# Kernel tuning notes

Hardware: AMD Instinct MI355X
Metric: run time of the kernel (lower is better)

The kernel has to match this reference:

```python
import jax, jax.numpy as jnp
import numpy as np

N_HEADS = 16


def _rope_table(seq_len, head_dim):
    # Matches RotaryPositionalEmbedding: emb = cat(sin(pos*inv_freq), cos(pos*inv_freq))
    inv_freq = 1.0 / (10000.0 ** (jnp.arange(0, head_dim, 2, dtype=jnp.float32) / head_dim))
    sinusoid = jnp.arange(seq_len, dtype=jnp.float32)[:, None] * inv_freq[None, :]  # [S, hd/2]
    return jnp.sin(sinusoid), jnp.cos(sinusoid)


def _apply_rope(q, k, seq_len, head_dim):
    # Faithful to the torch code, which slices emb[:, :hd/2] (== sin) and calls it 'cos',
    # and emb[:, hd/2:] (== cos) and calls it 'sin'. We keep that exact math.
    sin_tab, cos_tab = _rope_table(seq_len, head_dim)
    c = sin_tab[None, None]  # named 'cos' in torch code, actually sin values
    s = cos_tab[None, None]  # named 'sin' in torch code, actually cos values
    half = head_dim // 2
    def rot(x):
        x1, x2 = x[..., :half], x[..., half:]
        return jnp.concatenate([x1 * c - x2 * s, x2 * c + x1 * s], axis=-1)
    return rot(q), rot(k)


def setup_inputs() -> dict:
    key = jax.random.key(0)
    ks = jax.random.split(key, 9)
    B, S, D = 4, 2048, 1024
    sc = 1.0 / np.sqrt(D)
    return {
        'hidden_states': jax.random.normal(ks[0], (B, S, D), jnp.float32),
        'Wq': jax.random.normal(ks[1], (D, D), jnp.float32) * sc,
        'bq': jax.random.normal(ks[2], (D,), jnp.float32) * 0.01,
        'Wk': jax.random.normal(ks[3], (D, D), jnp.float32) * sc,
        'bk': jax.random.normal(ks[4], (D,), jnp.float32) * 0.01,
        'Wv': jax.random.normal(ks[5], (D, D), jnp.float32) * sc,
        'bv': jax.random.normal(ks[6], (D,), jnp.float32) * 0.01,
        'Wo': jax.random.normal(ks[7], (D, D), jnp.float32) * sc,
        'bo': jax.random.normal(ks[8], (D,), jnp.float32) * 0.01,
    }


def reference(hidden_states, Wq, bq, Wk, bk, Wv, bv, Wo, bo):
    B, S, D = hidden_states.shape
    H = N_HEADS
    hd = D // H

    def proj(W, b):
        y = jnp.einsum('bsd,ed->bse', hidden_states, W) + b  # nn.Linear: x @ W.T + b
        return y.reshape(B, S, H, hd).transpose(0, 2, 1, 3)   # [B,H,S,hd]

    q = proj(Wq, bq)
    k = proj(Wk, bk)
    v = proj(Wv, bv)
    q, k = _apply_rope(q, k, S, hd)

    scale = 1.0 / np.sqrt(hd)
    scores = jnp.einsum('bhqd,bhkd->bhqk', q, k) * scale  # [B,H,S,S]
    attn = jax.nn.softmax(scores, axis=-1)
    ctx = jnp.einsum('bhqk,bhkd->bhqd', attn, v)          # [B,H,S,hd]
    ctx = ctx.transpose(0, 2, 1, 3).reshape(B, S, D)
    return jnp.einsum('bsd,ed->bse', ctx, Wo) + bo
```

## Files before the change

kernel.cpp:

```cpp
#include <hip/hip_runtime.h>
#include <math.h>

#define SEQ 2048
#define DMODEL 1024
#define NH 16
#define HD 64
#define BH 64
#define MROWS 8192
#define QKV_U16 8388608
#define LOG2E 1.4426950408889634f

typedef __attribute__((ext_vector_type(8))) _Float16 half8;
typedef __attribute__((ext_vector_type(4))) _Float16 half4;
typedef __attribute__((ext_vector_type(2))) __fp16 fp16v2;
typedef __attribute__((ext_vector_type(8))) short short8;
typedef __attribute__((ext_vector_type(4))) float floatx4;
typedef unsigned short ush;

union FH { _Float16 h; ush u; };
union PK { fp16v2 v; unsigned u; };
union PH { unsigned u[2]; half4 h; };

__device__ inline ush f2h(float x) { FH c; c.h = (_Float16)x; return c.u; }

__device__ inline void glds16(const ush* g, ush* l) {
  __builtin_amdgcn_global_load_lds((const __attribute__((address_space(1))) void*)g,
                                   (__attribute__((address_space(3))) void*)l, 16, 0, 0);
}

__global__ __launch_bounds__(256)
void cvt_kb(const float* __restrict__ src, ush* __restrict__ dst, int M) {
  __shared__ float T[64][33];
  const int t = threadIdx.x;
  const int k0 = blockIdx.x * 32, m0 = blockIdx.y * 64;
  {
    int row = t >> 2, c = (t & 3) * 8;
    const float* sp = src + (size_t)(m0 + row) * DMODEL + k0 + c;
    float4 x0 = *(const float4*)sp;
    float4 x1 = *(const float4*)(sp + 4);
    float xs[8] = {x0.x, x0.y, x0.z, x0.w, x1.x, x1.y, x1.z, x1.w};
#pragma unroll
    for (int j = 0; j < 8; ++j) T[row][c + j] = xs[j];
  }
  __syncthreads();
  const int ml = t & 63, kbl = t >> 6;
  short8 h8;
#pragma unroll
  for (int j = 0; j < 8; ++j) h8[j] = (short)f2h(T[ml][kbl * 8 + j]);
  *(short8*)(dst + ((size_t)(k0 / 8 + kbl) * M + m0 + ml) * 8) = h8;
}

__global__ __launch_bounds__(256)
void cvt_w4(const float* __restrict__ W0, const float* __restrict__ W1,
            const float* __restrict__ W2, const float* __restrict__ W3,
            ush* __restrict__ dst, float2* __restrict__ tab) {
  __shared__ float T[64][33];
  const int z = blockIdx.z;
  if (z == 3) {
    const int idx = (blockIdx.y * 32 + blockIdx.x) * 256 + threadIdx.x;
    if (idx < 65536) {
      const int s = idx >> 5, i = idx & 31;
      const float f = (float)pow(10000.0, -(double)i / 32.0);
      const float ang = (float)s * f;
      tab[idx] = make_float2(sinf(ang), cosf(ang));
    }
  }
  const float* src = (z == 0) ? W0 : (z == 1) ? W1 : (z == 2) ? W2 : W3;
  ush* dz = dst + (size_t)z * DMODEL * DMODEL;
  const int t = threadIdx.x;
  const int k0 = blockIdx.x * 32, m0 = blockIdx.y * 64;
  {
    int row = t >> 2, c = (t & 3) * 8;
    const float* sp = src + (size_t)(m0 + row) * DMODEL + k0 + c;
    float4 x0 = *(const float4*)sp;
    float4 x1 = *(const float4*)(sp + 4);
    float xs[8] = {x0.x, x0.y, x0.z, x0.w, x1.x, x1.y, x1.z, x1.w};
#pragma unroll
    for (int j = 0; j < 8; ++j) T[row][c + j] = xs[j];
  }
  __syncthreads();
  const int ml = t & 63, kbl = t >> 6;
  short8 h8;
#pragma unroll
  for (int j = 0; j < 8; ++j) h8[j] = (short)f2h(T[ml][kbl * 8 + j]);
  *(short8*)(dz + ((size_t)(k0 / 8 + kbl) * DMODEL + m0 + ml) * 8) = h8;
}

template<int QKV>
__global__ __launch_bounds__(512, 2)
void gemm_f16(const ush* __restrict__ A, const ush* __restrict__ W0,
              const float* __restrict__ b0, const float* __restrict__ b1,
              const float* __restrict__ b2, void* __restrict__ out0,
              void* __restrict__ out1, void* __restrict__ out2,
              const float2* __restrict__ sctab) {
  constexpr int NT = 16;
  __shared__ ush SA[3][16384];
  __shared__ ush SW[3][8192];
  const int tid  = threadIdx.x;
  const int wave = tid >> 6;
  const int lane = tid & 63;
  const int fr = lane & 15;
  const int fg = lane >> 4;
  const int wm = wave >> 1;
  const int wn = wave & 1;

  const int zz = QKV ? (blockIdx.x >> 3) : 3;
  const int nx = QKV ? (blockIdx.x & 7) : blockIdx.x;
  const int m0 = blockIdx.y * 256;
  const int n0 = nx * 128;
  const int m_base = m0 + wm * 64;
  const int n_base = n0 + wn * 64;

  const ush* W = W0 + (size_t)(QKV ? zz : 0) * (DMODEL * DMODEL);
  const float* bias = QKV ? (zz == 0 ? b0 : zz == 1 ? b1 : b2) : b0;
  void* outp = QKV ? (zz == 0 ? out0 : zz == 1 ? out1 : out2) : out0;
  const float scale = (QKV && zz == 0) ? 0.125f * LOG2E : 1.0f;

  floatx4 acc[4][4];
#pragma unroll
  for (int i = 0; i < 4; ++i)
#pragma unroll
    for (int j = 0; j < 4; ++j) acc[i][j] = (floatx4){0.f, 0.f, 0.f, 0.f};

  auto stageA = [&](int b, int kt, int p) {
    const int c = p * 512 + wave * 64;
    const int kb = c >> 8, r0 = c & 255;
    glds16(A + (size_t)(kt * 8 + kb) * (MROWS * 8) + (size_t)(m0 + r0 + lane) * 8,
           &SA[b][(size_t)c * 8]);
  };
  auto stageB = [&](int b, int kt, int p) {
    const int c = p * 512 + wave * 64;
    const int kb = c >> 7, r0 = c & 127;
    glds16(W + (size_t)(kt * 8 + kb) * (DMODEL * 8) + (size_t)(n0 + r0 + lane) * 8,
           &SW[b][(size_t)c * 8]);
  };
  auto stageAll = [&](int b, int kt) {
    stageA(b, kt, 0); stageA(b, kt, 1); stageA(b, kt, 2); stageA(b, kt, 3);
    stageB(b, kt, 0); stageB(b, kt, 1);
  };

  auto doPhase = [&](int b, int kh, int b2, int t2, int which) {
    const int kbl = kh * 4 + fg;
    half8 ah[4], wh[4];
#pragma unroll
    for (int tm = 0; tm < 4; ++tm)
      ah[tm] = *(const half8*)&SA[b][(size_t)(kbl * 256 + wm * 64 + tm * 16 + fr) * 8];
#pragma unroll
    for (int tn = 0; tn < 4; ++tn)
      wh[tn] = *(const half8*)&SW[b][(size_t)(kbl * 128 + wn * 64 + tn * 16 + fr) * 8];
    if (which == 0 && t2 < NT) { stageA(b2, t2, 0); stageA(b2, t2, 1); stageA(b2, t2, 2); }
    if (which == 1 && t2 < NT) { stageA(b2, t2, 3); stageB(b2, t2, 0); stageB(b2, t2, 1); }
    __builtin_amdgcn_s_barrier();
    __builtin_amdgcn_sched_barrier(0);
    __builtin_amdgcn_s_setprio(1);
#pragma unroll
    for (int tm = 0; tm < 4; ++tm)
#pragma unroll
      for (int tn = 0; tn < 4; ++tn)
        acc[tm][tn] = __builtin_amdgcn_mfma_f32_16x16x32_f16(ah[tm], wh[tn], acc[tm][tn], 0, 0, 0);
    __builtin_amdgcn_s_setprio(0);
  };

  stageAll(0, 0);
  stageAll(1, 1);
  asm volatile("s_waitcnt vmcnt(6)" ::: "memory");
  __builtin_amdgcn_s_barrier();
  __builtin_amdgcn_sched_barrier(0);

  int bc = 0;
  for (int t = 0; t < NT; ++t) {
    int b2 = bc + 2; if (b2 >= 3) b2 -= 3;
    doPhase(bc, 0, b2, t + 2, 0);
    __builtin_amdgcn_s_barrier();
    __builtin_amdgcn_sched_barrier(0);
    doPhase(bc, 1, b2, t + 2, 1);
    if (t + 1 < NT) {
      if (t + 2 < NT) asm volatile("s_waitcnt vmcnt(6)" ::: "memory");
      else            asm volatile("s_waitcnt vmcnt(0)" ::: "memory");
      __builtin_amdgcn_s_barrier();
      __builtin_amdgcn_sched_barrier(0);
    }
    ++bc; if (bc == 3) bc = 0;
  }

  float bias_s[4];
#pragma unroll
  for (int tn = 0; tn < 4; ++tn) bias_s[tn] = bias[n_base + tn * 16 + fr];

  if (!QKV) {
#pragma unroll
    for (int tm = 0; tm < 4; ++tm)
#pragma unroll
      for (int tn = 0; tn < 4; ++tn)
#pragma unroll
        for (int r = 0; r < 4; ++r) {
          const int m = m_base + tm * 16 + fg * 4 + r;
          const int n = n_base + tn * 16 + fr;
          ((float*)outp)[(size_t)m * DMODEL + n] = acc[tm][tn][r] + bias_s[tn];
        }
    return;
  }

  const int h = (n_base >> 6) & 15;
  ush* out = (ush*)outp;

  if (zz == 2) {
#pragma unroll
    for (int tm = 0; tm < 4; ++tm)
#pragma unroll
      for (int tn = 0; tn < 4; ++tn)
#pragma unroll
        for (int r = 0; r < 4; ++r) {
          const int m = m_base + tm * 16 + fg * 4 + r;
          const int s = m & (SEQ - 1);
          const size_t bh = (size_t)((m >> 11) * NH + h);
          const int d = tn * 16 + fr;
          const int k6 = s & 63, ktl = s >> 6;
          const int s2 = k6 >> 5;
          const int jj = ((k6 >> 4) & 1) * 4 + (k6 & 3);
          const int fgv = (k6 >> 2) & 3;
          const int dt = d >> 4, frv = d & 15;
          size_t pos = ((((bh * 32 + ktl) * 4 + dt) * 2 + s2) * 64 + fgv * 16 + frv) * 8 + jj;
          out[pos] = f2h(acc[tm][tn][r] + bias_s[tn]);
        }
    return;
  }

#pragma unroll
  for (int tn2 = 0; tn2 < 2; ++tn2) {
    const int i = tn2 * 16 + fr;
#pragma unroll
    for (int tm = 0; tm < 4; ++tm)
#pragma unroll
      for (int r = 0; r < 4; ++r) {
        const int m = m_base + tm * 16 + fg * 4 + r;
        const int s = m & (SEQ - 1);
        const size_t bh = (size_t)((m >> 11) * NH + h);
        const float x1 = acc[tm][tn2][r] + bias_s[tn2];
        const float x2 = acc[tm][tn2 + 2][r] + bias_s[tn2 + 2];
        const float2 sc = sctab[(s << 5) + i];
        const float sv = sc.x, cv = sc.y;
        const float o1 = (x1 * sv - x2 * cv) * scale;
        const float o2 = (x2 * sv + x1 * cv) * scale;
        const int d1 = i, d2 = i + 32;
#pragma unroll
        for (int e = 0; e < 2; ++e) {
          const int d = e ? d2 : d1;
          const float ov = e ? o2 : o1;
          const int ks = d >> 5, fgq = (d >> 3) & 3, j = d & 7;
          size_t pos;
          if (zz == 0) {
            const int qt = s >> 5, mm = (s >> 4) & 1, fr2 = s & 15;
            pos = ((((bh * 64 + qt) * 2 + mm) * 2 + ks) * 64 + fgq * 16 + fr2) * 8 + j;
          } else {
            const int ktl = s >> 6, jt = (s >> 4) & 3, fr2 = s & 15;
            pos = ((((bh * 32 + ktl) * 4 + jt) * 2 + ks) * 64 + fgq * 16 + fr2) * 8 + j;
          }
          out[pos] = f2h(ov);
        }
      }
  }
}

__global__ __launch_bounds__(256, 2)
void flash_mfma(const ush* __restrict__ qsw, const ush* __restrict__ ksw,
                const ush* __restrict__ vsw, ush* __restrict__ ctxf) {
  __shared__ __align__(16) ush Tep[4][64][72];
  __shared__ float Lden[4][64];
  const int tid = threadIdx.x;
  const int wave = tid >> 6;
  const int lane = tid & 63;
  const int fr = lane & 15;
  const int fg = lane >> 4;

  const int lin = blockIdx.x + 8 * blockIdx.y;
  const int xcd = lin & 7;
  const int t2  = lin >> 3;
  const int qblk = t2 & 7;
  const int bh   = xcd + 8 * (t2 >> 3);

  const int q0 = qblk * 256 + wave * 64;
  const ush* qp = qsw + ((size_t)bh * 64 + (q0 >> 5)) * 2048;
  const ush* kp = ksw + (size_t)bh * 131072;
  const ush* vp = vsw + (size_t)bh * 131072;

  half8 qf[4][2];
#pragma unroll
  for (int qn = 0; qn < 4; ++qn)
#pragma unroll
    for (int ks = 0; ks < 2; ++ks)
      qf[qn][ks] = *(const half8*)(qp + (qn * 2 + ks) * 512 + lane * 8);

  floatx4 oacc[4][4];
#pragma unroll
  for (int qn = 0; qn < 4; ++qn)
#pragma unroll
    for (int i = 0; i < 4; ++i) oacc[qn][i] = (floatx4){0.f, 0.f, 0.f, 0.f};
  float lsum[4] = {0.f, 0.f, 0.f, 0.f};

  const fp16v2 one2 = {(__fp16)1.0f, (__fp16)1.0f};

#pragma unroll 2
  for (int kt = 0; kt < 32; ++kt) {
    const ush* ktp = kp + kt * 4096;
    const ush* vtp = vp + kt * 4096;

    half8 kf[8], vf[8];
#pragma unroll
    for (int i = 0; i < 8; ++i) kf[i] = *(const half8*)(ktp + i * 512 + lane * 8);
#pragma unroll
    for (int i = 0; i < 8; ++i) vf[i] = *(const half8*)(vtp + i * 512 + lane * 8);

#pragma unroll
    for (int qn = 0; qn < 4; ++qn) {
      floatx4 s4[4];
#pragma unroll
      for (int jt = 0; jt < 4; ++jt) s4[jt] = (floatx4){0.f, 0.f, 0.f, 0.f};
      __builtin_amdgcn_s_setprio(1);
#pragma unroll
      for (int ks = 0; ks < 2; ++ks)
#pragma unroll
        for (int jt = 0; jt < 4; ++jt)
          s4[jt] = __builtin_amdgcn_mfma_f32_16x16x32_f16(kf[jt * 2 + ks], qf[qn][ks], s4[jt], 0, 0, 0);
      __builtin_amdgcn_s_setprio(0);

      half4 P[4];
#pragma unroll
      for (int jt = 0; jt < 4; ++jt) {
        float p0 = __builtin_amdgcn_exp2f(s4[jt][0]);
        float p1 = __builtin_amdgcn_exp2f(s4[jt][1]);
        float p2 = __builtin_amdgcn_exp2f(s4[jt][2]);
        float p3 = __builtin_amdgcn_exp2f(s4[jt][3]);
        PK a, b;
        a.v = __builtin_amdgcn_cvt_pkrtz(p0, p1);
        b.v = __builtin_amdgcn_cvt_pkrtz(p2, p3);
        lsum[qn] = __builtin_amdgcn_fdot2(a.v, one2, lsum[qn], false);
        lsum[qn] = __builtin_amdgcn_fdot2(b.v, one2, lsum[qn], false);
        PH ph; ph.u[0] = a.u; ph.u[1] = b.u;
        P[jt] = ph.h;
      }

      __builtin_amdgcn_s_setprio(1);
#pragma unroll
      for (int s2 = 0; s2 < 2; ++s2) {
        half8 p8 = __builtin_shufflevector(P[s2 * 2], P[s2 * 2 + 1], 0, 1, 2, 3, 4, 5, 6, 7);
#pragma unroll
        for (int dt = 0; dt < 4; ++dt)
          oacc[qn][dt] = __builtin_amdgcn_mfma_f32_16x16x32_f16(p8, vf[dt * 2 + s2], oacc[qn][dt], 0, 0, 0);
      }
      __builtin_amdgcn_s_setprio(0);
    }
  }

#pragma unroll
  for (int qn = 0; qn < 4; ++qn) {
    lsum[qn] += __shfl_xor(lsum[qn], 16);
    lsum[qn] += __shfl_xor(lsum[qn], 32);
    Lden[wave][qn * 16 + fr] = lsum[qn];
  }

  const int b = bh >> 4, h = bh & 15;
#pragma unroll
  for (int qn = 0; qn < 4; ++qn)
#pragma unroll
    for (int r = 0; r < 4; ++r) {
      const float inv = 1.0f / Lden[wave][qn * 16 + fg * 4 + r];
#pragma unroll
      for (int dt = 0; dt < 4; ++dt)
        Tep[wave][qn * 16 + fg * 4 + r][dt * 16 + fr] = f2h(oacc[qn][dt][r] * inv);
    }
  const size_t mrow0 = (size_t)b * SEQ + q0;
  const int kb = lane >> 3;
#pragma unroll
  for (int i = 0; i < 8; ++i) {
    const int q = (lane & 7) + i * 8;
    short8 v = *(const short8*)&Tep[wave][q][kb * 8];
    *(short8*)(ctxf + ((size_t)(h * 8 + kb) * MROWS + mrow0 + q) * 8) = v;
  }
}

extern "C" void kernel_launch(void* const* d_in, const int* in_sizes, int n_in,
                              void* d_out, int out_size, void* d_ws, size_t ws_size,
                              hipStream_t stream) {
  const float* hs = (const float*)d_in[0];
  const float* Wq = (const float*)d_in[1];
  const float* bq = (const float*)d_in[2];
  const float* Wk = (const float*)d_in[3];
  const float* bk = (const float*)d_in[4];
  const float* Wv = (const float*)d_in[5];
  const float* bv = (const float*)d_in[6];
  const float* Wo = (const float*)d_in[7];
  const float* bo = (const float*)d_in[8];

  ush* qsw  = (ush*)d_ws;
  ush* ksw  = qsw + QKV_U16;
  ush* vsw  = ksw + QKV_U16;
  ush* hsf  = vsw + QKV_U16;
  ush* ctxf = hsf + QKV_U16;
  ush* Wf4  = ctxf + QKV_U16;
  float2* sctab = (float2*)(Wf4 + 4 * DMODEL * DMODEL);

  const size_t WS = (size_t)DMODEL * DMODEL;

  cvt_w4<<<dim3(32, 16, 4), 256, 0, stream>>>(Wq, Wk, Wv, Wo, Wf4, sctab);
  cvt_kb<<<dim3(32, 128), 256, 0, stream>>>(hs, hsf, MROWS);

  gemm_f16<1><<<dim3(24, 32), 512, 0, stream>>>(hsf, Wf4, bq, bk, bv,
                                                qsw, ksw, vsw, sctab);

  flash_mfma<<<dim3(8, BH), 256, 0, stream>>>(qsw, ksw, vsw, ctxf);

  gemm_f16<0><<<dim3(8, 32), 512, 0, stream>>>(ctxf, Wf4 + 3 * WS, bo, nullptr, nullptr,
                                               d_out, nullptr, nullptr, sctab);
}
```

Measured before the change: 260.0 us.

## Split attention over two KV halves and merge partial outputs in a combine kernel

New measurement: 544.7 us. 110% more time.

```diff
diff --git a/kernel.cpp b/kernel.cpp
--- a/kernel.cpp
+++ b/kernel.cpp
@@ -22,6 +22,7 @@
 union PH { unsigned u[2]; half4 h; };
 
 __device__ inline ush f2h(float x) { FH c; c.h = (_Float16)x; return c.u; }
+__device__ inline float h2f(ush u) { FH c; c.u = u; return (float)c.h; }
 
 __device__ inline void glds16(const ush* g, ush* l) {
   __builtin_amdgcn_global_load_lds((const __attribute__((address_space(1))) void*)g,
@@ -262,9 +263,10 @@
   }
 }
 
-__global__ __launch_bounds__(256, 2)
+__global__ __launch_bounds__(256, 4)
 void flash_mfma(const ush* __restrict__ qsw, const ush* __restrict__ ksw,
-                const ush* __restrict__ vsw, ush* __restrict__ ctxf) {
+                const ush* __restrict__ vsw, ush* __restrict__ ctxf,
+                ush* __restrict__ part1, float* __restrict__ Lbuf) {
   __shared__ __align__(16) ush Tep[4][64][72];
   __shared__ float Lden[4][64];
   const int tid = threadIdx.x;
@@ -278,6 +280,7 @@
   const int t2  = lin >> 3;
   const int qblk = t2 & 7;
   const int bh   = xcd + 8 * (t2 >> 3);
+  const int z    = blockIdx.z;
 
   const int q0 = qblk * 256 + wave * 64;
   const ush* qp = qsw + ((size_t)bh * 64 + (q0 >> 5)) * 2048;
@@ -300,8 +303,9 @@
 
   const fp16v2 one2 = {(__fp16)1.0f, (__fp16)1.0f};
 
+  const int kt0 = z * 16;
 #pragma unroll 2
-  for (int kt = 0; kt < 32; ++kt) {
+  for (int kt = kt0; kt < kt0 + 16; ++kt) {
     const ush* ktp = kp + kt * 4096;
     const ush* vtp = vp + kt * 4096;
 
@@ -357,8 +361,11 @@
     lsum[qn] += __shfl_xor(lsum[qn], 16);
     lsum[qn] += __shfl_xor(lsum[qn], 32);
     Lden[wave][qn * 16 + fr] = lsum[qn];
-  }
-
+    if (fg == 0)
+      Lbuf[(size_t)z * 131072 + (size_t)bh * 2048 + q0 + qn * 16 + fr] = lsum[qn];
+  }
+
+  ush* dst = z ? part1 : ctxf;
   const int b = bh >> 4, h = bh & 15;
 #pragma unroll
   for (int qn = 0; qn < 4; ++qn)
@@ -375,8 +382,31 @@
   for (int i = 0; i < 8; ++i) {
     const int q = (lane & 7) + i * 8;
     short8 v = *(const short8*)&Tep[wave][q][kb * 8];
-    *(short8*)(ctxf + ((size_t)(h * 8 + kb) * MROWS + mrow0 + q) * 8) = v;
-  }
+    *(short8*)(dst + ((size_t)(h * 8 + kb) * MROWS + mrow0 + q) * 8) = v;
+  }
+}
+
+__global__ __launch_bounds__(256)
+void combine_ctx(ush* __restrict__ ctxf, const ush* __restrict__ part1,
+                 const float* __restrict__ Lbuf) {
+  const size_t c = (size_t)blockIdx.x * 256 + threadIdx.x;
+  const int kbk = (int)(c >> 13);
+  const int mrow = (int)(c & 8191);
+  const int h = kbk >> 3;
+  const int b = mrow >> 11;
+  const int s = mrow & 2047;
+  const size_t li = (size_t)(b * 16 + h) * 2048 + s;
+  const float L0 = Lbuf[li];
+  const float L1 = Lbuf[131072 + li];
+  const float w0 = L0 / (L0 + L1);
+  const float w1 = 1.0f - w0;
+  short8 a = *(const short8*)(ctxf + c * 8);
+  short8 p = *(const short8*)(part1 + c * 8);
+  short8 o;
+#pragma unroll
+  for (int j = 0; j < 8; ++j)
+    o[j] = (short)f2h(h2f((ush)a[j]) * w0 + h2f((ush)p[j]) * w1);
+  *(short8*)(ctxf + c * 8) = o;
 }
 
 extern "C" void kernel_launch(void* const* d_in, const int* in_sizes, int n_in,
@@ -399,6 +429,7 @@
   ush* ctxf = hsf + QKV_U16;
   ush* Wf4  = ctxf + QKV_U16;
   float2* sctab = (float2*)(Wf4 + 4 * DMODEL * DMODEL);
+  float* Lbuf = (float*)(sctab + 65536);
 
   const size_t WS = (size_t)DMODEL * DMODEL;
 
@@ -408,7 +439,8 @@
   gemm_f16<1><<<dim3(24, 32), 512, 0, stream>>>(hsf, Wf4, bq, bk, bv,
                                                 qsw, ksw, vsw, sctab);
 
-  flash_mfma<<<dim3(8, BH), 256, 0, stream>>>(qsw, ksw, vsw, ctxf);
+  flash_mfma<<<dim3(8, BH, 2), 256, 0, stream>>>(qsw, ksw, vsw, ctxf, hsf, Lbuf);
+  combine_ctx<<<4096, 256, 0, stream>>>(ctxf, hsf, Lbuf);
 
   gemm_f16<0><<<dim3(8, 32), 512, 0, stream>>>(ctxf, Wf4 + 3 * WS, bo, nullptr, nullptr,
                                                d_out, nullptr, nullptr, sctab);
```
